# Kernel optimization log

Hardware: AMD Instinct MI355X
Metric: run time of the kernel (lower is better)

Reference implementation:

```python
import jax, jax.numpy as jnp
jax.config.update('jax_enable_x64', True)
import numpy as np

B = 16          # samples per batch
PTS = 50000     # points per sample
PP = 2048       # pairs per sample
C = 64          # backbone_out_channels
HID = 1024      # mlp_hidden
MASK = 65535
RANK_MSE_WEIGHT = 0.1


def _hash4(idx):
    # pack (b, x, y, z) into one int64 key, 16 bits per field
    idx = idx.astype(jnp.int64)
    return ((idx[:, 0] & MASK) << 48) | ((idx[:, 1] & MASK) << 32) | ((idx[:, 2] & MASK) << 16) | (idx[:, 3] & MASK)


def setup_inputs() -> dict:
    key = jax.random.key(0)
    ks = jax.random.split(key, 8)
    N = B * PTS
    P = B * PP
    grid_coord = jax.random.randint(ks[0], (N, 3), 0, 1024, dtype=jnp.int32)
    offset = (jnp.arange(1, B + 1) * PTS).astype(jnp.int64)          # cumulative point ends
    batch = jnp.searchsorted(offset, jnp.arange(N), side='right')
    point_indices = jnp.concatenate([batch[:, None].astype(jnp.int32), grid_coord], axis=1)
    perm = jax.random.permutation(ks[1], N)
    voxel_indices = point_indices[perm].astype(jnp.int64)            # backbone._last_indices
    voxel_features = jax.random.normal(ks[2], (N, C), dtype=jnp.float32)
    pairs = jax.random.randint(ks[3], (P, 2), 0, PTS, dtype=jnp.int64)   # sample-local indices
    pair_reward = jax.random.uniform(ks[4], (P,), dtype=jnp.float32)
    pair_offset = (jnp.arange(1, B + 1) * PP).astype(jnp.int64)      # cumulative pair ends
    din = 3 * C
    def lin(k, fi, fo):
        return jax.random.normal(k, (fi, fo), dtype=jnp.float32) / np.float32(np.sqrt(fi))
    W1 = lin(ks[5], din, HID); b1 = jnp.zeros((HID,), jnp.float32)
    W2 = lin(ks[6], HID, HID); b2 = jnp.zeros((HID,), jnp.float32)
    W3 = lin(ks[7], HID, 1);   b3 = jnp.zeros((1,), jnp.float32)
    return dict(voxel_features=voxel_features, pair_reward=pair_reward,
                W1=W1, b1=b1, W2=W2, b2=b2, W3=W3, b3=b3,
                grid_coord=grid_coord, offset=offset, voxel_indices=voxel_indices,
                pairs=pairs, pair_offset=pair_offset)


def reference(voxel_features, pair_reward, W1, b1, W2, b2, W3, b3,
              grid_coord, offset, voxel_indices, pairs, pair_offset):
    N = grid_coord.shape[0]
    # --- match sparse voxel features back to point order (sort + searchsorted + gather) ---
    batch = jnp.searchsorted(offset, jnp.arange(N), side='right')
    point_keys = _hash4(jnp.concatenate([batch[:, None].astype(jnp.int32), grid_coord], axis=1))
    voxel_keys = _hash4(voxel_indices)
    order = jnp.argsort(voxel_keys)
    vk_sorted = voxel_keys[order]
    loc = jnp.clip(jnp.searchsorted(vk_sorted, point_keys), 0, N - 1)
    point_feat = voxel_features[order[loc]]                          # [N, C]
    # --- shift sample-local pair indices by per-sample point start (vectorized offsets) ---
    P = pairs.shape[0]
    seg = jnp.searchsorted(pair_offset, jnp.arange(P), side='right') # segment id per pair
    point_starts = jnp.concatenate([jnp.zeros((1,), offset.dtype), offset[:-1]])
    shifted = pairs + point_starts[seg][:, None]
    f0 = point_feat[shifted[:, 0]]
    f1 = point_feat[shifted[:, 1]]
    pair_feat = jnp.concatenate([f0, f1, f0 - f1], axis=1)           # [P, 3C]
    # --- MLP head ---
    h = jax.nn.relu(pair_feat @ W1 + b1)
    h = jax.nn.relu(h @ W2 + b2)
    pred = (h @ W3 + b3)[:, 0]                                       # [P]
    # --- pair_rank loss, batched over equal-sized segments ---
    Bn = pair_offset.shape[0]
    Pp = P // Bn
    pb = pred.reshape(Bn, Pp)
    tb = pair_reward.reshape(Bn, Pp)
    dp = pb[:, :, None] - pb[:, None, :]                             # [B, Pp, Pp]
    dt = tb[:, :, None] - tb[:, None, :]
    sgn = jnp.sign(dt)
    triu = jnp.triu(jnp.ones((Pp, Pp), bool), 1)
    valid = triu[None, :, :] & (sgn != 0)
    sp = jax.nn.softplus(-sgn * dp)
    cnt = valid.sum(axis=(1, 2))
    rank_per = jnp.where(valid, sp, 0.0).sum(axis=(1, 2)) / jnp.maximum(cnt, 1)
    has = cnt > 0
    rank_loss = jnp.where(has, rank_per, 0.0).sum() / jnp.maximum(has.sum(), 1)
    mse_loss = jnp.mean((pb - tb) ** 2, axis=1).mean()
    loss = rank_loss + RANK_MSE_WEIGHT * mse_loss
    return loss
```

## Files before the change

kernel.cpp:

```cpp
#include <hip/hip_runtime.h>
#include <stdint.h>

#define BATCH   16
#define PTS     50000
#define PP      2048
#define NPTS    (BATCH*PTS)
#define NPAIR   (BATCH*PP)
#define NEND    (2*NPAIR)
#define CFEAT   64
#define KIN     128
#define HID     1024
#define QTS_LOG2 17
#define QTS     (1u<<QTS_LOG2)
#define QTS_MASK (QTS-1)
#define EMPTY_KEY 0xFFFFFFFFFFFFFFFFULL
#define NJB     64
#define RJ      (PP/NJB)

typedef unsigned long long ull;
typedef __attribute__((ext_vector_type(4))) float f32x4;
typedef __attribute__((ext_vector_type(8))) short bf16x8;

__device__ __forceinline__ ull mix64(ull h) {
  h ^= h >> 33; h *= 0xff51afd7ed558ccdULL;
  h ^= h >> 33; h *= 0xc4ceb9fe1a85ec53ULL;
  h ^= h >> 33; return h;
}

__device__ __forceinline__ unsigned short f2b(float x) {
  unsigned u = __float_as_uint(x);
  unsigned r = (u + 0x7FFFu + ((u >> 16) & 1u)) >> 16;
  return (unsigned short)r;
}

__global__ __launch_bounds__(256) void setup_kernel(
    ull* __restrict__ qtable, unsigned int* __restrict__ ans,
    const float* __restrict__ W1, unsigned short* __restrict__ Wt1,
    const float* __restrict__ W2, unsigned short* __restrict__ Wt2) {
  __shared__ unsigned short tile[32][33];
  int bid = blockIdx.x;
  int t = threadIdx.x;
  if (bid < 512) {
    int i = bid * 256 + t;
    qtable[i] = EMPTY_KEY;
    ans[i] = 0xFFFFFFFFu;
  } else if (bid < 1024) {
    int idx = (bid - 512) * 256 + t;
    int n = idx >> 7, k = idx & 127;
    float v;
    if (k < 64)
      v = W1[(size_t)k * HID + n] + W1[(size_t)(128 + k) * HID + n];
    else
      v = W1[(size_t)k * HID + n] - W1[(size_t)(64 + k) * HID + n];
    Wt1[(size_t)n * KIN + k] = f2b(v);
  } else {
    int b = bid - 1024;
    int nb = (b & 31) * 32, kb = (b >> 5) * 32;
    int tx = t & 31, ty = t >> 5;
#pragma unroll
    for (int r = 0; r < 32; r += 8)
      tile[ty + r][tx] = f2b(W2[(size_t)(kb + ty + r) * HID + nb + tx]);
    __syncthreads();
#pragma unroll
    for (int r = 0; r < 32; r += 8)
      Wt2[(size_t)(nb + ty + r) * HID + kb + tx] = tile[tx][ty + r];
  }
}

__global__ void qinsert(const int* __restrict__ pairs, const int* __restrict__ gc,
                        ull* __restrict__ qtable, unsigned int* __restrict__ eslot) {
  int e = blockIdx.x * blockDim.x + threadIdx.x;
  if (e >= NEND) return;
  int j = e >> 1, side = e & 1;
  int seg = j / PP;
  int pi = pairs[2*j + side] + seg * PTS;
  pi = pi < 0 ? 0 : (pi >= NPTS ? NPTS - 1 : pi);
  ull key = ((ull)seg << 30) | ((ull)(gc[3*pi] & 1023) << 20)
          | ((ull)(gc[3*pi+1] & 1023) << 10) | (ull)(gc[3*pi+2] & 1023);
  unsigned int h = (unsigned int)mix64(key) & QTS_MASK;
  for (int p = 0; p < (int)QTS; ++p) {
    ull prev = atomicCAS(&qtable[h], EMPTY_KEY, key);
    if (prev == EMPTY_KEY || prev == key) { eslot[e] = h; return; }
    h = (h + 1) & QTS_MASK;
  }
  eslot[e] = 0;
}

__global__ void vscan(const int* __restrict__ vidx, const ull* __restrict__ qtable,
                      unsigned int* __restrict__ ans) {
  int i = blockIdx.x * blockDim.x + threadIdx.x;
  if (i >= NPTS) return;
  int4 v = *(const int4*)&vidx[4*i];
  ull key = ((ull)(v.x & 31) << 30) | ((ull)(v.y & 1023) << 20)
          | ((ull)(v.z & 1023) << 10) | (ull)(v.w & 1023);
  unsigned int h = (unsigned int)mix64(key) & QTS_MASK;
  for (int p = 0; p < (int)QTS; ++p) {
    ull k = qtable[h];
    if (k == key) { atomicMin(&ans[h], (unsigned int)i); return; }
    if (k == EMPTY_KEY) return;
    h = (h + 1) & QTS_MASK;
  }
}

__global__ void gatherA(const float* __restrict__ vf,
                        const unsigned int* __restrict__ eslot,
                        const unsigned int* __restrict__ ans,
                        int jbase, unsigned short* __restrict__ Ab, int mrows) {
  int idx = blockIdx.x * 256 + threadIdx.x;
  if (idx >= mrows * 32) return;
  int j = idx >> 5, c4 = (idx & 31) * 4;
  int side = (c4 < 64) ? 0 : 1;
  unsigned int r = ans[eslot[2 * (jbase + j) + side]];
  r = r < (unsigned)NPTS ? r : 0u;
  int c = (c4 < 64) ? c4 : (c4 - 64);
  float4 v = *(const float4*)&vf[(size_t)r * CFEAT + c];
  ushort4 o;
  o.x = f2b(v.x); o.y = f2b(v.y); o.z = f2b(v.z); o.w = f2b(v.w);
  *(ushort4*)&Ab[(size_t)j * KIN + c4] = o;
}

template<bool FUSE>
__global__ __launch_bounds__(256) void gemm_mfma(
    const unsigned short* __restrict__ Ab, const unsigned short* __restrict__ Bt,
    const float* __restrict__ bias, const float* __restrict__ W3,
    unsigned short* __restrict__ Cb, float* __restrict__ partial,
    int M, int N, int K) {
  __shared__ unsigned short As[128 * 64];
  __shared__ unsigned short Bs[128 * 64];
  int t = threadIdx.x;
  int lane = t & 63, w = t >> 6;
  int l15 = lane & 15, lhi = lane >> 4;
  int wm = w >> 1, wn = w & 1;
  int ncol = gridDim.x;
  int stripe, cb;
  if ((gridDim.y & 7) == 0) {
    int h = blockIdx.x + ncol * blockIdx.y;
    stripe = (h & 7) + 8 * (h / (8 * ncol));
    cb = (h >> 3) % ncol;
  } else {
    stripe = blockIdx.y; cb = blockIdx.x;
  }
  int row0 = stripe * 128, col0 = cb * 128;
  size_t Kb = (size_t)K * 2;
  f32x4 acc[4][4] = {};
  const char* Ac = (const char*)As;
  const char* Bc = (const char*)Bs;
  for (int k0 = 0; k0 < K; k0 += 64) {
#pragma unroll
    for (int it = 0; it < 4; ++it) {
      int q = (it * 4 + w) * 64 + lane;
      int row = q >> 3, slot = q & 7;
      int sb = (slot * 16) ^ ((row & 7) << 4);
      const char* gA = (const char*)Ab + (size_t)(row0 + row) * Kb + (size_t)k0 * 2 + sb;
      const char* gB = (const char*)Bt + (size_t)(col0 + row) * Kb + (size_t)k0 * 2 + sb;
      char* lA = (char*)As + (it * 4 + w) * 1024;
      char* lB = (char*)Bs + (it * 4 + w) * 1024;
      __builtin_amdgcn_global_load_lds((const __attribute__((address_space(1))) void*)gA,
                                       (__attribute__((address_space(3))) void*)lA, 16, 0, 0);
      __builtin_amdgcn_global_load_lds((const __attribute__((address_space(1))) void*)gB,
                                       (__attribute__((address_space(3))) void*)lB, 16, 0, 0);
    }
    __syncthreads();
#pragma unroll
    for (int s = 0; s < 2; ++s) {
      bf16x8 af[4], bfr[4];
#pragma unroll
      for (int mi = 0; mi < 4; ++mi) {
        int row = wm * 64 + mi * 16 + l15;
        int off = row * 128 + ((s * 64 + lhi * 16) ^ ((row & 7) << 4));
        af[mi] = *(const bf16x8*)(Ac + off);
      }
#pragma unroll
      for (int ni = 0; ni < 4; ++ni) {
        int row = wn * 64 + ni * 16 + l15;
        int off = row * 128 + ((s * 64 + lhi * 16) ^ ((row & 7) << 4));
        bfr[ni] = *(const bf16x8*)(Bc + off);
      }
#pragma unroll
      for (int mi = 0; mi < 4; ++mi)
#pragma unroll
        for (int ni = 0; ni < 4; ++ni)
          acc[mi][ni] = __builtin_amdgcn_mfma_f32_16x16x32_bf16(af[mi], bfr[ni], acc[mi][ni], 0, 0, 0);
    }
    __syncthreads();
  }
  if (!FUSE) {
#pragma unroll
    for (int ni = 0; ni < 4; ++ni) {
      int col = col0 + wn * 64 + ni * 16 + l15;
      float bv = bias[col];
#pragma unroll
      for (int mi = 0; mi < 4; ++mi)
#pragma unroll
        for (int r = 0; r < 4; ++r) {
          int row = row0 + wm * 64 + mi * 16 + lhi * 4 + r;
          Cb[(size_t)row * N + col] = f2b(fmaxf(acc[mi][ni][r] + bv, 0.f));
        }
    }
  } else {
    float bb[4], ww[4];
#pragma unroll
    for (int ni = 0; ni < 4; ++ni) {
      int col = col0 + wn * 64 + ni * 16 + l15;
      bb[ni] = bias[col];
      ww[ni] = W3[col];
    }
#pragma unroll
    for (int mi = 0; mi < 4; ++mi)
#pragma unroll
      for (int r = 0; r < 4; ++r) {
        float pv = 0.f;
#pragma unroll
        for (int ni = 0; ni < 4; ++ni)
          pv += fmaxf(acc[mi][ni][r] + bb[ni], 0.f) * ww[ni];
        pv += __shfl_xor(pv, 1);
        pv += __shfl_xor(pv, 2);
        pv += __shfl_xor(pv, 4);
        pv += __shfl_xor(pv, 8);
        if (l15 == 0) {
          int row = row0 + wm * 64 + mi * 16 + lhi * 4 + r;
          partial[(size_t)row * 16 + cb * 2 + wn] = pv;
        }
      }
  }
}

#define BARF() do { asm volatile("" ::: "memory"); __builtin_amdgcn_s_barrier(); \
                    asm volatile("" ::: "memory"); } while (0)
#define Q_MFMA(MIB, NIB)                                                         \
  do {                                                                           \
    __builtin_amdgcn_s_setprio(1);                                               \
    _Pragma("unroll")                                                            \
    for (int mi = 0; mi < 4; ++mi)                                               \
      _Pragma("unroll")                                                          \
      for (int ni = 0; ni < 2; ++ni)                                             \
        _Pragma("unroll")                                                        \
        for (int s = 0; s < 2; ++s)                                              \
          acc[(MIB)*4 + mi][(NIB)*2 + ni] = __builtin_amdgcn_mfma_f32_16x16x32_bf16( \
              af[mi][s], bfr[(NIB)*2 + ni][s], acc[(MIB)*4 + mi][(NIB)*2 + ni], 0, 0, 0); \
    __builtin_amdgcn_s_setprio(0);                                               \
  } while (0)

__global__ __launch_bounds__(512, 2) void gemm2_8phase(
    const unsigned short* __restrict__ Ab, const unsigned short* __restrict__ Bt,
    const float* __restrict__ bias, const float* __restrict__ W3,
    float* __restrict__ partial, int M, int N, int K) {
  __shared__ char SM[131072];
  const int t = threadIdx.x;
  const int lane = t & 63;
  const int w = t >> 6;
  const int l15 = lane & 15, lhi = lane >> 4;
  const int wm = w >> 2, wn = w & 3;
  const int ncol = gridDim.x;
  const int h = blockIdx.x + ncol * blockIdx.y;
  const int stripe = (h & 7) + 8 * (h / (8 * ncol));
  const int cb = (h >> 3) % ncol;
  const int row0 = stripe * 256, col0 = cb * 256;
  const size_t Kb = (size_t)K * 2;
  const int nt = K >> 6;

  f32x4 acc[8][4] = {};

  auto STA = [&](int bq, int qa, int kt) {
    int rho = t >> 3, slot = t & 7;
    const char* g = (const char*)Ab + (size_t)(row0 + qa * 64 + rho) * Kb
                    + (size_t)kt * 128 + ((slot * 16) ^ ((rho & 7) << 4));
    char* l = SM + bq * 32768 + qa * 8192 + t * 16;
    __builtin_amdgcn_global_load_lds((const __attribute__((address_space(1))) void*)g,
                                     (__attribute__((address_space(3))) void*)l, 16, 0, 0);
  };
  auto STB = [&](int bq, int qb, int kt) {
    int rho = t >> 3, slot = t & 7;
    const char* g = (const char*)Bt + (size_t)(col0 + qb * 64 + rho) * Kb
                    + (size_t)kt * 128 + ((slot * 16) ^ ((rho & 7) << 4));
    char* l = SM + 65536 + bq * 32768 + qb * 8192 + t * 16;
    __builtin_amdgcn_global_load_lds((const __attribute__((address_space(1))) void*)g,
                                     (__attribute__((address_space(3))) void*)l, 16, 0, 0);
  };
  auto LDA = [&](int bq, int mi, int s) -> bf16x8 {
    int r = wm * 128 + mi * 16 + l15;
    int rho = r & 63;
    return *(const bf16x8*)(SM + bq * 32768 + (r >> 6) * 8192 + rho * 128
                            + ((s * 64 + lhi * 16) ^ ((rho & 7) << 4)));
  };
  auto LDB = [&](int bq, int ni, int s) -> bf16x8 {
    int r = wn * 64 + ni * 16 + l15;
    int rho = r & 63;
    return *(const bf16x8*)(SM + 65536 + bq * 32768 + (r >> 6) * 8192 + rho * 128
                            + ((s * 64 + lhi * 16) ^ ((rho & 7) << 4)));
  };

  STA(0, 0, 0); STA(0, 2, 0); STB(0, 0, 0); STB(0, 1, 0);
  STA(0, 1, 0); STA(0, 3, 0); STB(0, 2, 0); STB(0, 3, 0);
  if (nt > 1) { STA(1, 0, 1); STA(1, 2, 1); STB(1, 0, 1); STB(1, 1, 1);
                STA(1, 1, 1); STA(1, 3, 1); }
  asm volatile("s_waitcnt vmcnt(6)" ::: "memory");
  __builtin_amdgcn_s_barrier();
  asm volatile("" ::: "memory");

  bf16x8 af[4][2], bfr[4][2];
  for (int tt = 0; tt < nt; ++tt) {
    const int bq = tt & 1, nb = bq ^ 1;
#pragma unroll
    for (int mi = 0; mi < 4; ++mi)
#pragma unroll
      for (int s = 0; s < 2; ++s) af[mi][s] = LDA(bq, mi, s);
#pragma unroll
    for (int ni = 0; ni < 4; ++ni)
#pragma unroll
      for (int s = 0; s < 2; ++s) bfr[ni][s] = LDB(bq, ni, s);
    if (tt + 1 < nt) { STB(nb, 2, tt + 1); STB(nb, 3, tt + 1); }
    BARF();
    Q_MFMA(0, 0);
    BARF();
    if (tt + 2 < nt) { STA(bq, 0, tt + 2); STA(bq, 2, tt + 2); }
    BARF();
    Q_MFMA(0, 1);
    BARF();
#pragma unroll
    for (int mi = 0; mi < 4; ++mi)
#pragma unroll
      for (int s = 0; s < 2; ++s) af[mi][s] = LDA(bq, 4 + mi, s);
    if (tt + 2 < nt) { STB(bq, 0, tt + 2); STB(bq, 1, tt + 2); }
    BARF();
    Q_MFMA(1, 0);
    BARF();
    if (tt + 2 < nt) { STA(bq, 1, tt + 2); STA(bq, 3, tt + 2); }
    BARF();
    Q_MFMA(1, 1);
    asm volatile("s_waitcnt vmcnt(6)" ::: "memory");
    BARF();
  }

  float bb[4], ww[4];
#pragma unroll
  for (int ni = 0; ni < 4; ++ni) {
    int col = col0 + wn * 64 + ni * 16 + l15;
    bb[ni] = bias[col];
    ww[ni] = W3[col];
  }
#pragma unroll
  for (int mi = 0; mi < 8; ++mi)
#pragma unroll
    for (int r = 0; r < 4; ++r) {
      float pv = 0.f;
#pragma unroll
      for (int ni = 0; ni < 4; ++ni)
        pv += fmaxf(acc[mi][ni][r] + bb[ni], 0.f) * ww[ni];
      pv += __shfl_xor(pv, 1);
      pv += __shfl_xor(pv, 2);
      pv += __shfl_xor(pv, 4);
      pv += __shfl_xor(pv, 8);
      if (l15 == 0) {
        int row = row0 + wm * 128 + mi * 16 + lhi * 4 + r;
        partial[(size_t)row * 16 + cb * 4 + wn] = pv;
      }
    }
}

__global__ void pred_kernel(const float* __restrict__ partial,
                            const float* __restrict__ b3, float* __restrict__ pred) {
  int j = blockIdx.x * blockDim.x + threadIdx.x;
  if (j >= NPAIR) return;
  float s = b3[0];
#pragma unroll
  for (int nb = 0; nb < 16; ++nb) s += partial[(size_t)j * 16 + nb];
  pred[j] = s;
}

__global__ __launch_bounds__(256) void rank_kernel(
    const float* __restrict__ pred, const float* __restrict__ rew,
    double* __restrict__ rank_part, unsigned int* __restrict__ cnt_part,
    double* __restrict__ mse_part) {
  int b = blockIdx.x;
  int jb = blockIdx.y;
  __shared__ float pb[PP];
  __shared__ float tb[PP];
  int t = threadIdx.x;
  for (int i = t; i < PP; i += 256) {
    pb[i] = pred[b * PP + i];
    tb[i] = rew[b * PP + i];
  }
  __syncthreads();
  float tj[RJ], pj[RJ];
  int j0 = jb * RJ;
#pragma unroll
  for (int r = 0; r < RJ; ++r) { tj[r] = tb[j0 + r]; pj[r] = pb[j0 + r]; }
  float fs = 0.f;
  unsigned int c = 0;
  for (int i = t; i < PP; i += 256) {
    float ti = tb[i], pi = pb[i];
#pragma unroll
    for (int r = 0; r < RJ; ++r) {
      float dt = ti - tj[r];
      float dp = pi - pj[r];
      float z = dt > 0.f ? -dp : dp;
      float e = __expf(-fabsf(z));
      float sp = fmaxf(z, 0.f) + __logf(1.f + e);
      bool v = dt != 0.f;
      fs += v ? sp : 0.f;
      c += v ? 1u : 0u;
    }
  }
  float msep = 0.f;
  if (jb == 0) {
    for (int i = t; i < PP; i += 256) {
      float d = pb[i] - tb[i];
      msep = fmaf(d, d, msep);
    }
  }
  __shared__ double sred[256];
  __shared__ unsigned int cred[256];
  __shared__ float mred[256];
  sred[t] = (double)fs; cred[t] = c; mred[t] = msep;
  __syncthreads();
  for (int off = 128; off > 0; off >>= 1) {
    if (t < off) {
      sred[t] += sred[t + off];
      cred[t] += cred[t + off];
      mred[t] += mred[t + off];
    }
    __syncthreads();
  }
  if (t == 0) {
    rank_part[b * NJB + jb] = sred[0];
    cnt_part[b * NJB + jb] = cred[0];
    if (jb == 0) mse_part[b] = (double)mred[0];
  }
}

__global__ void finalize_kernel(const double* __restrict__ rank_part,
                                const unsigned int* __restrict__ cnt_part,
                                const double* __restrict__ mse_part,
                                float* __restrict__ out) {
  __shared__ double rls[16];
  __shared__ double mss[16];
  __shared__ int hasv[16];
  int t = threadIdx.x;
  if (t < BATCH) {
    double s = 0.0;
    ull c = 0;
    for (int jb = 0; jb < NJB; ++jb) {
      s += rank_part[t * NJB + jb];
      c += cnt_part[t * NJB + jb];
    }
    rls[t] = c > 0 ? s / (double)c : 0.0;
    hasv[t] = c > 0 ? 1 : 0;
    mss[t] = mse_part[t] / (double)PP;
  }
  __syncthreads();
  if (t == 0) {
    double rl = 0.0, ms = 0.0;
    int has = 0;
    for (int b = 0; b < BATCH; ++b) { rl += rls[b]; has += hasv[b]; ms += mss[b]; }
    double rank_loss = rl / (double)(has > 0 ? has : 1);
    double mse_loss = ms / (double)BATCH;
    out[0] = (float)(rank_loss + 0.1 * mse_loss);
  }
}

extern "C" void kernel_launch(void* const* d_in, const int* in_sizes, int n_in,
                              void* d_out, int out_size, void* d_ws, size_t ws_size,
                              hipStream_t stream) {
  const float* vf   = (const float*)d_in[0];
  const float* rew  = (const float*)d_in[1];
  const float* W1   = (const float*)d_in[2];
  const float* b1   = (const float*)d_in[3];
  const float* W2   = (const float*)d_in[4];
  const float* b2   = (const float*)d_in[5];
  const float* W3   = (const float*)d_in[6];
  const float* b3   = (const float*)d_in[7];
  const int*   gc   = (const int*)d_in[8];
  const int*   vidx  = (const int*)d_in[10];
  const int*   pairs = (const int*)d_in[11];

  char* ws = (char*)d_ws;
  size_t off = 0;
  auto alloc = [&](size_t bytes) -> void* {
    void* p = ws + off;
    off += (bytes + 255) & ~(size_t)255;
    return p;
  };
  ull* qtable          = (ull*)alloc((size_t)QTS * 8);
  unsigned int* eslot  = (unsigned int*)alloc((size_t)NEND * 4);
  unsigned int* ans    = (unsigned int*)alloc((size_t)QTS * 4);
  float* partial       = (float*)alloc((size_t)NPAIR * 16 * 4);
  float* pred          = (float*)alloc((size_t)NPAIR * 4);
  double* rank_part    = (double*)alloc((size_t)BATCH * NJB * 8);
  unsigned int* cnt_p  = (unsigned int*)alloc((size_t)BATCH * NJB * 4);
  double* mse_part     = (double*)alloc((size_t)BATCH * 8);
  unsigned short* Wt1  = (unsigned short*)alloc((size_t)HID * KIN * 2);
  unsigned short* Wt2  = (unsigned short*)alloc((size_t)HID * HID * 2);

  int mchunk = 2048;
  for (int cand = NPAIR; cand >= 2048; cand >>= 1) {
    size_t need = off + (size_t)cand * (KIN * 2 + HID * 2) + 2 * 65536;
    if (need <= ws_size) { mchunk = cand; break; }
  }
  unsigned short* Ab = (unsigned short*)alloc((size_t)mchunk * KIN * 2);
  unsigned short* h1 = (unsigned short*)alloc((size_t)mchunk * HID * 2);

  setup_kernel<<<2048, 256, 0, stream>>>(qtable, ans, W1, Wt1, W2, Wt2);
  qinsert<<<(NEND + 255) / 256, 256, 0, stream>>>(pairs, gc, qtable, eslot);
  vscan<<<(NPTS + 255) / 256, 256, 0, stream>>>(vidx, qtable, ans);

  int nchunk = NPAIR / mchunk;
  for (int ch = 0; ch < nchunk; ++ch) {
    gatherA<<<(mchunk * 32 + 255) / 256, 256, 0, stream>>>(
        vf, eslot, ans, ch * mchunk, Ab, mchunk);
    dim3 g1(HID / 128, mchunk / 128);
    gemm_mfma<false><<<g1, 256, 0, stream>>>(Ab, Wt1, b1, nullptr, h1, nullptr,
                                             mchunk, HID, KIN);
    if (mchunk >= 512 && (mchunk & 255) == 0) {
      dim3 g2(HID / 256, mchunk / 256);
      gemm2_8phase<<<g2, 512, 0, stream>>>(h1, Wt2, b2, W3,
                                           partial + (size_t)ch * mchunk * 16,
                                           mchunk, HID, HID);
    } else {
      dim3 g2(HID / 128, mchunk / 128);
      gemm_mfma<true><<<g2, 256, 0, stream>>>(h1, Wt2, b2, W3, nullptr,
                                              partial + (size_t)ch * mchunk * 16,
                                              mchunk, HID, HID);
    }
  }

  pred_kernel<<<(NPAIR + 255) / 256, 256, 0, stream>>>(partial, b3, pred);
  rank_kernel<<<dim3(BATCH, NJB), 256, 0, stream>>>(pred, rew, rank_part, cnt_p, mse_part);
  finalize_kernel<<<1, 64, 0, stream>>>(rank_part, cnt_p, mse_part, (float*)d_out);
}
```

Before: 199.2 us.

## Fuse pair feature gather into first GEMM and fold pred sum into rank kernel

```diff
diff --git a/kernel.cpp b/kernel.cpp
--- a/kernel.cpp
+++ b/kernel.cpp
@@ -99,6 +99,94 @@
     if (k == key) { atomicMin(&ans[h], (unsigned int)i); return; }
     if (k == EMPTY_KEY) return;
     h = (h + 1) & QTS_MASK;
+  }
+}
+
+__global__ __launch_bounds__(256) void gemm1_fused(
+    const float* __restrict__ vf, const unsigned int* __restrict__ eslot,
+    const unsigned int* __restrict__ ans, const unsigned short* __restrict__ Bt,
+    const float* __restrict__ bias, unsigned short* __restrict__ Cb, int M) {
+  __shared__ unsigned short As[128 * 64];
+  __shared__ unsigned short Bs[128 * 64];
+  int t = threadIdx.x;
+  int lane = t & 63, w = t >> 6;
+  int l15 = lane & 15, lhi = lane >> 4;
+  int wm = w >> 1, wn = w & 1;
+  int ncol = gridDim.x;
+  int stripe, cb;
+  if ((gridDim.y & 7) == 0) {
+    int h = blockIdx.x + ncol * blockIdx.y;
+    stripe = (h & 7) + 8 * (h / (8 * ncol));
+    cb = (h >> 3) % ncol;
+  } else {
+    stripe = blockIdx.y; cb = blockIdx.x;
+  }
+  int row0 = stripe * 128, col0 = cb * 128;
+  const size_t Kb = (size_t)KIN * 2;
+  f32x4 acc[4][4] = {};
+  const char* Ac = (const char*)As;
+  const char* Bc = (const char*)Bs;
+  int arow = t >> 1, ahalf = t & 1;
+#pragma unroll
+  for (int kt = 0; kt < 2; ++kt) {
+    unsigned int rr = ans[eslot[2 * (row0 + arow) + kt]];
+    rr = rr < (unsigned)NPTS ? rr : 0u;
+    const float* src = vf + (size_t)rr * CFEAT + ahalf * 32;
+    char* adst = (char*)As + arow * 128;
+    int aswz = (arow & 7) << 4;
+#pragma unroll
+    for (int i = 0; i < 8; ++i) {
+      float4 v = *(const float4*)(src + 4 * i);
+      ull o = (ull)f2b(v.x) | ((ull)f2b(v.y) << 16)
+            | ((ull)f2b(v.z) << 32) | ((ull)f2b(v.w) << 48);
+      *(ull*)(adst + ((ahalf * 64 + 8 * i) ^ aswz)) = o;
+    }
+#pragma unroll
+    for (int it = 0; it < 4; ++it) {
+      int q = (it * 4 + w) * 64 + lane;
+      int brow = q >> 3, slot = q & 7;
+      int sb = (slot * 16) ^ ((brow & 7) << 4);
+      const char* gB = (const char*)Bt + (size_t)(col0 + brow) * Kb
+                     + (size_t)kt * 128 + sb;
+      char* lB = (char*)Bs + (it * 4 + w) * 1024;
+      __builtin_amdgcn_global_load_lds((const __attribute__((address_space(1))) void*)gB,
+                                       (__attribute__((address_space(3))) void*)lB, 16, 0, 0);
+    }
+    __syncthreads();
+#pragma unroll
+    for (int s = 0; s < 2; ++s) {
+      bf16x8 af[4], bfr[4];
+#pragma unroll
+      for (int mi = 0; mi < 4; ++mi) {
+        int row = wm * 64 + mi * 16 + l15;
+        int off = row * 128 + ((s * 64 + lhi * 16) ^ ((row & 7) << 4));
+        af[mi] = *(const bf16x8*)(Ac + off);
+      }
+#pragma unroll
+      for (int ni = 0; ni < 4; ++ni) {
+        int row = wn * 64 + ni * 16 + l15;
+        int off = row * 128 + ((s * 64 + lhi * 16) ^ ((row & 7) << 4));
+        bfr[ni] = *(const bf16x8*)(Bc + off);
+      }
+#pragma unroll
+      for (int mi = 0; mi < 4; ++mi)
+#pragma unroll
+        for (int ni = 0; ni < 4; ++ni)
+          acc[mi][ni] = __builtin_amdgcn_mfma_f32_16x16x32_bf16(af[mi], bfr[ni], acc[mi][ni], 0, 0, 0);
+    }
+    __syncthreads();
+  }
+#pragma unroll
+  for (int ni = 0; ni < 4; ++ni) {
+    int col = col0 + wn * 64 + ni * 16 + l15;
+    float bv = bias[col];
+#pragma unroll
+    for (int mi = 0; mi < 4; ++mi)
+#pragma unroll
+      for (int r = 0; r < 4; ++r) {
+        int row = row0 + wm * 64 + mi * 16 + lhi * 4 + r;
+        Cb[(size_t)row * HID + col] = f2b(fmaxf(acc[mi][ni][r] + bv, 0.f));
+      }
   }
 }
 
@@ -358,18 +446,9 @@
     }
 }
 
-__global__ void pred_kernel(const float* __restrict__ partial,
-                            const float* __restrict__ b3, float* __restrict__ pred) {
-  int j = blockIdx.x * blockDim.x + threadIdx.x;
-  if (j >= NPAIR) return;
-  float s = b3[0];
-#pragma unroll
-  for (int nb = 0; nb < 16; ++nb) s += partial[(size_t)j * 16 + nb];
-  pred[j] = s;
-}
-
 __global__ __launch_bounds__(256) void rank_kernel(
-    const float* __restrict__ pred, const float* __restrict__ rew,
+    const float* __restrict__ partial, const float* __restrict__ b3,
+    const float* __restrict__ rew,
     double* __restrict__ rank_part, unsigned int* __restrict__ cnt_part,
     double* __restrict__ mse_part) {
   int b = blockIdx.x;
@@ -377,8 +456,13 @@
   __shared__ float pb[PP];
   __shared__ float tb[PP];
   int t = threadIdx.x;
+  float b3v = b3[0];
   for (int i = t; i < PP; i += 256) {
-    pb[i] = pred[b * PP + i];
+    float s = b3v;
+    const float* pr = &partial[(size_t)(b * PP + i) * 16];
+#pragma unroll
+    for (int nb = 0; nb < 16; ++nb) s += pr[nb];
+    pb[i] = s;
     tb[i] = rew[b * PP + i];
   }
   __syncthreads();
@@ -485,7 +569,6 @@
   unsigned int* eslot  = (unsigned int*)alloc((size_t)NEND * 4);
   unsigned int* ans    = (unsigned int*)alloc((size_t)QTS * 4);
   float* partial       = (float*)alloc((size_t)NPAIR * 16 * 4);
-  float* pred          = (float*)alloc((size_t)NPAIR * 4);
   double* rank_part    = (double*)alloc((size_t)BATCH * NJB * 8);
   unsigned int* cnt_p  = (unsigned int*)alloc((size_t)BATCH * NJB * 4);
   double* mse_part     = (double*)alloc((size_t)BATCH * 8);
@@ -497,34 +580,41 @@
     size_t need = off + (size_t)cand * (KIN * 2 + HID * 2) + 2 * 65536;
     if (need <= ws_size) { mchunk = cand; break; }
   }
-  unsigned short* Ab = (unsigned short*)alloc((size_t)mchunk * KIN * 2);
   unsigned short* h1 = (unsigned short*)alloc((size_t)mchunk * HID * 2);
 
   setup_kernel<<<2048, 256, 0, stream>>>(qtable, ans, W1, Wt1, W2, Wt2);
   qinsert<<<(NEND + 255) / 256, 256, 0, stream>>>(pairs, gc, qtable, eslot);
   vscan<<<(NPTS + 255) / 256, 256, 0, stream>>>(vidx, qtable, ans);
 
-  int nchunk = NPAIR / mchunk;
-  for (int ch = 0; ch < nchunk; ++ch) {
-    gatherA<<<(mchunk * 32 + 255) / 256, 256, 0, stream>>>(
-        vf, eslot, ans, ch * mchunk, Ab, mchunk);
-    dim3 g1(HID / 128, mchunk / 128);
-    gemm_mfma<false><<<g1, 256, 0, stream>>>(Ab, Wt1, b1, nullptr, h1, nullptr,
-                                             mchunk, HID, KIN);
-    if (mchunk >= 512 && (mchunk & 255) == 0) {
-      dim3 g2(HID / 256, mchunk / 256);
-      gemm2_8phase<<<g2, 512, 0, stream>>>(h1, Wt2, b2, W3,
-                                           partial + (size_t)ch * mchunk * 16,
-                                           mchunk, HID, HID);
-    } else {
-      dim3 g2(HID / 128, mchunk / 128);
-      gemm_mfma<true><<<g2, 256, 0, stream>>>(h1, Wt2, b2, W3, nullptr,
-                                              partial + (size_t)ch * mchunk * 16,
-                                              mchunk, HID, HID);
-    }
-  }
-
-  pred_kernel<<<(NPAIR + 255) / 256, 256, 0, stream>>>(partial, b3, pred);
-  rank_kernel<<<dim3(BATCH, NJB), 256, 0, stream>>>(pred, rew, rank_part, cnt_p, mse_part);
+  if (mchunk == NPAIR) {
+    dim3 g1(HID / 128, NPAIR / 128);
+    gemm1_fused<<<g1, 256, 0, stream>>>(vf, eslot, ans, Wt1, b1, h1, NPAIR);
+    dim3 g2(HID / 256, NPAIR / 256);
+    gemm2_8phase<<<g2, 512, 0, stream>>>(h1, Wt2, b2, W3, partial, NPAIR, HID, HID);
+  } else {
+    unsigned short* Ab = (unsigned short*)alloc((size_t)mchunk * KIN * 2);
+    int nchunk = NPAIR / mchunk;
+    for (int ch = 0; ch < nchunk; ++ch) {
+      gatherA<<<(mchunk * 32 + 255) / 256, 256, 0, stream>>>(
+          vf, eslot, ans, ch * mchunk, Ab, mchunk);
+      dim3 g1(HID / 128, mchunk / 128);
+      gemm_mfma<false><<<g1, 256, 0, stream>>>(Ab, Wt1, b1, nullptr, h1, nullptr,
+                                               mchunk, HID, KIN);
+      if (mchunk >= 512 && (mchunk & 255) == 0) {
+        dim3 g2(HID / 256, mchunk / 256);
+        gemm2_8phase<<<g2, 512, 0, stream>>>(h1, Wt2, b2, W3,
+                                             partial + (size_t)ch * mchunk * 16,
+                                             mchunk, HID, HID);
+      } else {
+        dim3 g2(HID / 128, mchunk / 128);
+        gemm_mfma<true><<<g2, 256, 0, stream>>>(h1, Wt2, b2, W3, nullptr,
+                                                partial + (size_t)ch * mchunk * 16,
+                                                mchunk, HID, HID);
+      }
+    }
+  }
+
+  rank_kernel<<<dim3(BATCH, NJB), 256, 0, stream>>>(partial, b3, rew,
+                                                    rank_part, cnt_p, mse_part);
   finalize_kernel<<<1, 64, 0, stream>>>(rank_part, cnt_p, mse_part, (float*)d_out);
 }
```

New measurement: 206.0 us. 1.03x slower.
